# Optimization experiments

Measured on AMD Instinct MI355X. Metric: run time of the kernel, lower is better.

## Reference

```python
import jax, jax.numpy as jnp
import numpy as np

EPS_DEN = 1e-7
EPS_SQRT = 1e-12  # clamp before sqrt (torch.cdist matmul-mode also clamps at 0)


def setup_inputs() -> dict:
    key = jax.random.key(0)
    k1, k2 = jax.random.split(key)
    L, N, Q, C = 6, 256, 64, 256
    hs_pair = jax.random.normal(k1, (L, N, Q, C), dtype=jnp.float32)
    centers = jax.random.normal(k2, (L, N, 2, C), dtype=jnp.float32)
    return {"hs_pair": hs_pair, "centers": centers}


def reference(hs_pair, centers):
    # hs_pair: [L, N, Q, C], centers: [L, N, 2, C]
    L, N, Q, C = hs_pair.shape
    x2 = jnp.sum(hs_pair * hs_pair, axis=-1)  # [L, N, Q], constant over iters

    def body(carry, _):
        cen, _prev_a = carry
        c2 = jnp.sum(cen * cen, axis=-1)                     # [L, N, 2]
        xc = jnp.einsum('lnqc,lnkc->lnqk', hs_pair, cen)     # [L, N, Q, 2]
        d2 = x2[..., None] + c2[:, :, None, :] - 2.0 * xc
        dist = jnp.sqrt(jnp.maximum(d2, EPS_SQRT))           # euclidean cdist
        a = jax.nn.softmax(-dist, axis=-1)                   # [L, N, Q, 2]
        num = jnp.einsum('lnqk,lnqc->lnkc', a, hs_pair)      # [L, N, 2, C]
        den = jnp.sum(a, axis=2)                             # [L, N, 2]
        new_cen = num / (den[..., None] + EPS_DEN)
        return (new_cen, a), None

    init_a = jnp.zeros((L, N, Q, 2), dtype=hs_pair.dtype)
    # Q sequential EM iterations; final assignment is the one computed from
    # the centers *before* the last update (matches the torch loop order).
    (centers_out, assignment), _ = jax.lax.scan(body, (centers, init_a), None, length=Q)
    return centers_out, assignment
```

## Files before the change

kernel.cpp:

```cpp
#include <hip/hip_runtime.h>

namespace {
constexpr int PB = 6 * 256;
constexpr int Q = 64;
constexpr int C = 256;
constexpr float EPS_DEN = 1e-7f;
constexpr float EPS_SQRT = 1e-12f;
constexpr int GT_FLOATS = Q * Q;
constexpr int AUX_FLOATS = 256;

typedef __attribute__((ext_vector_type(8))) short bf16x8;
typedef __attribute__((ext_vector_type(4))) float f32x4;

template <int CTRL>
__device__ __forceinline__ float ror_add(float v) {
  int r = __builtin_amdgcn_mov_dpp(__float_as_int(v), CTRL, 0xF, 0xF, true);
  return v + __int_as_float(r);
}

__device__ __forceinline__ float wave_total(float v) {
  v = ror_add<0x121>(v);
  v = ror_add<0x122>(v);
  v = ror_add<0x124>(v);
  v = ror_add<0x128>(v);
  {
    int t = __builtin_amdgcn_update_dpp(0, __float_as_int(v), 0x142, 0xA, 0xF,
                                        true);
    v = v + __int_as_float(t);
  }
  {
    int t = __builtin_amdgcn_update_dpp(0, __float_as_int(v), 0x143, 0xC, 0xF,
                                        true);
    v = v + __int_as_float(t);
  }
  return __int_as_float(__builtin_amdgcn_readlane(__float_as_int(v), 63));
}

__device__ __forceinline__ ushort bf16_rne(float x) {
  uint u = __float_as_uint(x);
  return (ushort)((u + 0x7FFFu + ((u >> 16) & 1u)) >> 16);
}
__device__ __forceinline__ float bf16_up(ushort h) {
  return __uint_as_float((uint)h << 16);
}

__device__ __forceinline__ void wave_fence() { asm volatile("" ::: "memory"); }
}

__global__ __launch_bounds__(256, 2) void k1_gram(
    const float* __restrict__ hs, const float* __restrict__ cen,
    float* __restrict__ ws) {
  const int prob = blockIdx.x;
  const int tid = threadIdx.x;
  const int lane = tid & 63, w = tid >> 6;
  const int li = lane & 15, lk = lane >> 4;

  __shared__ __align__(16) ushort Hh[64 * 128];
  __shared__ __align__(16) ushort Hl[64 * 128];
  __shared__ __align__(16) ushort Ch[2 * 256];
  __shared__ __align__(16) ushort Cl[2 * 256];

  const float4* hsg4 = (const float4*)(hs + (size_t)prob * Q * C);
  float* gtp = ws + (size_t)prob * GT_FLOATS;
  float* aux = ws + (size_t)PB * GT_FLOATS + (size_t)prob * AUX_FLOATS;

  f32x4 acc[4] = {{0.f, 0.f, 0.f, 0.f},
                  {0.f, 0.f, 0.f, 0.f},
                  {0.f, 0.f, 0.f, 0.f},
                  {0.f, 0.f, 0.f, 0.f}};
  f32x4 accX = {0.f, 0.f, 0.f, 0.f};
  const int rA = 16 * w + li;
  const int swz = (li & 7) << 4;

#pragma unroll 1
  for (int half = 0; half < 2; ++half) {
#pragma unroll
    for (int i = 0; i < 8; ++i) {
      const int c = i * 256 + tid;
      const int r = c >> 5, col4 = c & 31;
      float4 v = hsg4[r * 64 + half * 32 + col4];
      ushort h0 = bf16_rne(v.x), h1 = bf16_rne(v.y), h2 = bf16_rne(v.z),
             h3 = bf16_rne(v.w);
      ushort l0 = bf16_rne(v.x - bf16_up(h0));
      ushort l1 = bf16_rne(v.y - bf16_up(h1));
      ushort l2 = bf16_rne(v.z - bf16_up(h2));
      ushort l3 = bf16_rne(v.w - bf16_up(h3));
      const int boff = (col4 * 8) ^ ((r & 7) << 4);
      const int idx = r * 128 + (boff >> 1);
      *(ushort4*)&Hh[idx] = make_ushort4(h0, h1, h2, h3);
      *(ushort4*)&Hl[idx] = make_ushort4(l0, l1, l2, l3);
    }
    if (half == 0) {
      if (tid < 128) {
        const float4* cg4 = (const float4*)(cen + (size_t)prob * 2 * C);
        float4 v = cg4[tid];
        ushort h0 = bf16_rne(v.x), h1 = bf16_rne(v.y), h2 = bf16_rne(v.z),
               h3 = bf16_rne(v.w);
        ushort l0 = bf16_rne(v.x - bf16_up(h0));
        ushort l1 = bf16_rne(v.y - bf16_up(h1));
        ushort l2 = bf16_rne(v.z - bf16_up(h2));
        ushort l3 = bf16_rne(v.w - bf16_up(h3));
        const int idx = (tid >> 6) * 256 + (tid & 63) * 4;
        *(ushort4*)&Ch[idx] = make_ushort4(h0, h1, h2, h3);
        *(ushort4*)&Cl[idx] = make_ushort4(l0, l1, l2, l3);
      }
      float c0v = cen[(size_t)prob * 2 * C + tid];
      float c1v = cen[(size_t)prob * 2 * C + C + tid];
      float p0 = wave_total(c0v * c0v);
      float p1 = wave_total(c1v * c1v);
      if (lane == 0) {
        aux[192 + w] = p0;
        aux[196 + w] = p1;
      }
    }
    __syncthreads();

#pragma unroll
    for (int kk2 = 0; kk2 < 4; ++kk2) {
      const int kk = half * 4 + kk2;
      const int byteA = (kk2 * 64 + lk * 16) ^ swz;
      const int offA = byteA >> 1;
      bf16x8 ah = *(const bf16x8*)&Hh[rA * 128 + offA];
      bf16x8 al = *(const bf16x8*)&Hl[rA * 128 + offA];
      bf16x8 cbh = {0, 0, 0, 0, 0, 0, 0, 0};
      bf16x8 cbl = {0, 0, 0, 0, 0, 0, 0, 0};
      if (li < 2) {
        const int cidx = li * 256 + kk * 32 + lk * 8;
        cbh = *(const bf16x8*)&Ch[cidx];
        cbl = *(const bf16x8*)&Cl[cidx];
      }
      accX = __builtin_amdgcn_mfma_f32_16x16x32_bf16(ah, cbh, accX, 0, 0, 0);
      accX = __builtin_amdgcn_mfma_f32_16x16x32_bf16(ah, cbl, accX, 0, 0, 0);
      accX = __builtin_amdgcn_mfma_f32_16x16x32_bf16(al, cbh, accX, 0, 0, 0);
#pragma unroll
      for (int tj = 0; tj < 4; ++tj) {
        if (tj < w) continue;
        const int rB = 16 * tj + li;
        bf16x8 bh = *(const bf16x8*)&Hh[rB * 128 + offA];
        bf16x8 bl = *(const bf16x8*)&Hl[rB * 128 + offA];
        acc[tj] =
            __builtin_amdgcn_mfma_f32_16x16x32_bf16(ah, bh, acc[tj], 0, 0, 0);
        acc[tj] =
            __builtin_amdgcn_mfma_f32_16x16x32_bf16(ah, bl, acc[tj], 0, 0, 0);
        acc[tj] =
            __builtin_amdgcn_mfma_f32_16x16x32_bf16(al, bh, acc[tj], 0, 0, 0);
      }
    }
    __syncthreads();
  }

#pragma unroll
  for (int tj = 0; tj < 4; ++tj) {
    if (tj < w) continue;
#pragma unroll
    for (int r = 0; r < 4; ++r) {
      const float v = acc[tj][r];
      const int row = 16 * w + lk * 4 + r;
      const int col = 16 * tj + li;
      gtp[(col >> 2) * 256 + row * 4 + (col & 3)] = v;
      if (tj > w) gtp[(row >> 2) * 256 + col * 4 + (row & 3)] = v;
      if (row == col) aux[128 + row] = v;
    }
  }
  if (li < 2) {
#pragma unroll
    for (int r = 0; r < 4; ++r) {
      const int q = 16 * w + lk * 4 + r;
      aux[q * 2 + li] = accX[r];
    }
  }
}

__global__ __launch_bounds__(64, 2) void k2_iter(const float* __restrict__ hs,
                                                 const float* __restrict__ ws,
                                                 float* __restrict__ out) {
  const int prob = blockIdx.x;
  const int lane = threadIdx.x;
  const int li = lane & 15, lk = lane >> 4;

  __shared__ __align__(16) ushort Ah[2][64];
  __shared__ __align__(16) float m_s[2][64];
  __shared__ __align__(16) float a_s[2 * Q];

  const float4* gt4 = (const float4*)(ws + (size_t)prob * GT_FLOATS);
  const float* aux = ws + (size_t)PB * GT_FLOATS + (size_t)prob * AUX_FLOATS;

  bf16x8 Gh[4][2], Gl[4][2];
#pragma unroll
  for (int t = 0; t < 4; ++t) {
#pragma unroll
    for (int kk = 0; kk < 2; ++kk) {
      const int cj = 8 * kk + 2 * lk;
      float4 ga = gt4[cj * 64 + 16 * t + li];
      float4 gb = gt4[(cj + 1) * 64 + 16 * t + li];
      float g[8] = {ga.x, ga.y, ga.z, ga.w, gb.x, gb.y, gb.z, gb.w};
      bf16x8 hh, ll;
#pragma unroll
      for (int j = 0; j < 8; ++j) {
        ushort h = bf16_rne(g[j]);
        hh[j] = (short)h;
        ll[j] = (short)bf16_rne(g[j] - bf16_up(h));
      }
      Gh[t][kk] = hh;
      Gl[t][kk] = ll;
    }
  }

  const float x2 = aux[128 + lane];
  float xc0 = aux[lane * 2 + 0];
  float xc1 = aux[lane * 2 + 1];
  float c20 = aux[192] + aux[193] + aux[194] + aux[195];
  float c21 = aux[196] + aux[197] + aux[198] + aux[199];

  float a0 = 0.f, a1 = 0.f;
  const int cl = li & 1;

#pragma unroll 1
  for (int t = 0; t < Q; ++t) {
    float d0 = fmaxf(x2 + c20 - 2.f * xc0, EPS_SQRT);
    float d1 = fmaxf(x2 + c21 - 2.f * xc1, EPS_SQRT);
    float t0 = __builtin_amdgcn_sqrtf(d0), t1 = __builtin_amdgcn_sqrtf(d1);
    float e0 = __expf(-t0), e1 = __expf(-t1);
    float inv = __builtin_amdgcn_rcpf(e0 + e1);
    a0 = e0 * inv;
    a1 = e1 * inv;
    if (t == Q - 1) break;

    Ah[0][lane] = bf16_rne(a0);
    Ah[1][lane] = bf16_rne(a1);
    float den0 = wave_total(a0);
    float den1 = wave_total(a1);
    wave_fence();

    bf16x8 bh[2];
#pragma unroll
    for (int kk = 0; kk < 2; ++kk)
      bh[kk] = *(const bf16x8*)&Ah[cl][kk * 32 + lk * 8];

    f32x4 acc[4] = {{0.f, 0.f, 0.f, 0.f},
                    {0.f, 0.f, 0.f, 0.f},
                    {0.f, 0.f, 0.f, 0.f},
                    {0.f, 0.f, 0.f, 0.f}};
#pragma unroll
    for (int tt = 0; tt < 4; ++tt) {
#pragma unroll
      for (int kk = 0; kk < 2; ++kk) {
        acc[tt] = __builtin_amdgcn_mfma_f32_16x16x32_bf16(Gh[tt][kk], bh[kk],
                                                          acc[tt], 0, 0, 0);
        acc[tt] = __builtin_amdgcn_mfma_f32_16x16x32_bf16(Gl[tt][kk], bh[kk],
                                                          acc[tt], 0, 0, 0);
      }
    }
    if (li < 2) {
#pragma unroll
      for (int tt = 0; tt < 4; ++tt)
        *(float4*)&m_s[li][16 * tt + lk * 4] =
            make_float4(acc[tt][0], acc[tt][1], acc[tt][2], acc[tt][3]);
    }
    wave_fence();

    float m0 = m_s[0][lane];
    float m1 = m_s[1][lane];
    float s0 = wave_total(a0 * m0);
    float s1 = wave_total(a1 * m1);

    float i0 = __builtin_amdgcn_rcpf(den0 + EPS_DEN);
    float i1 = __builtin_amdgcn_rcpf(den1 + EPS_DEN);
    xc0 = m0 * i0;
    xc1 = m1 * i1;
    c20 = s0 * i0 * i0;
    c21 = s1 * i1 * i1;
  }

  *(float2*)&a_s[lane * 2] = make_float2(a0, a1);
  float den0 = wave_total(a0);
  float den1 = wave_total(a1);
  wave_fence();
  float i0 = __builtin_amdgcn_rcpf(den0 + EPS_DEN);
  float i1 = __builtin_amdgcn_rcpf(den1 + EPS_DEN);

  const float4* hb4 = (const float4*)(hs + (size_t)prob * Q * C);
  const float2* a2 = (const float2*)a_s;
  float4 n0 = make_float4(0.f, 0.f, 0.f, 0.f);
  float4 n1 = make_float4(0.f, 0.f, 0.f, 0.f);
#pragma unroll 8
  for (int q2 = 0; q2 < Q; ++q2) {
    float4 h = hb4[q2 * 64 + lane];
    float2 aq = a2[q2];
    n0.x = fmaf(aq.x, h.x, n0.x);
    n0.y = fmaf(aq.x, h.y, n0.y);
    n0.z = fmaf(aq.x, h.z, n0.z);
    n0.w = fmaf(aq.x, h.w, n0.w);
    n1.x = fmaf(aq.y, h.x, n1.x);
    n1.y = fmaf(aq.y, h.y, n1.y);
    n1.z = fmaf(aq.y, h.z, n1.z);
    n1.w = fmaf(aq.y, h.w, n1.w);
  }
  float4* outc4 = (float4*)(out + (size_t)prob * 2 * C);
  outc4[lane] = make_float4(n0.x * i0, n0.y * i0, n0.z * i0, n0.w * i0);
  outc4[64 + lane] = make_float4(n1.x * i1, n1.y * i1, n1.z * i1, n1.w * i1);

  float* outa = out + (size_t)PB * 2 * C + (size_t)prob * Q * 2;
  *(float2*)&outa[lane * 2] = make_float2(a0, a1);
}

extern "C" void kernel_launch(void* const* d_in, const int* in_sizes, int n_in,
                              void* d_out, int out_size, void* d_ws,
                              size_t ws_size, hipStream_t stream) {
  const float* hs = (const float*)d_in[0];
  const float* cen = (const float*)d_in[1];
  float* out = (float*)d_out;
  float* ws = (float*)d_ws;
  hipLaunchKernelGGL(k1_gram, dim3(PB), dim3(256), 0, stream, hs, cen, ws);
  hipLaunchKernelGGL(k2_iter, dim3(PB), dim3(64), 0, stream, hs, ws, out);
}
```

Before: 81.14 us.

## Load Gram-kernel MFMA operands directly from global memory, dropping LDS staging

```diff
diff --git a/kernel.cpp b/kernel.cpp
--- a/kernel.cpp
+++ b/kernel.cpp
@@ -44,6 +44,17 @@
   return __uint_as_float((uint)h << 16);
 }
 
+__device__ __forceinline__ void cvt8(float4 x, float4 y, bf16x8& hh,
+                                     bf16x8& ll) {
+  float v[8] = {x.x, x.y, x.z, x.w, y.x, y.y, y.z, y.w};
+#pragma unroll
+  for (int j = 0; j < 8; ++j) {
+    ushort h = bf16_rne(v[j]);
+    hh[j] = (short)h;
+    ll[j] = (short)bf16_rne(v[j] - bf16_up(h));
+  }
+}
+
 __device__ __forceinline__ void wave_fence() { asm volatile("" ::: "memory"); }
 }
 
@@ -55,14 +66,21 @@
   const int lane = tid & 63, w = tid >> 6;
   const int li = lane & 15, lk = lane >> 4;
 
-  __shared__ __align__(16) ushort Hh[64 * 128];
-  __shared__ __align__(16) ushort Hl[64 * 128];
-  __shared__ __align__(16) ushort Ch[2 * 256];
-  __shared__ __align__(16) ushort Cl[2 * 256];
-
-  const float4* hsg4 = (const float4*)(hs + (size_t)prob * Q * C);
+  const float* __restrict__ hsb = hs + (size_t)prob * Q * C;
+  const float* __restrict__ cenb = cen + (size_t)prob * 2 * C;
   float* gtp = ws + (size_t)prob * GT_FLOATS;
   float* aux = ws + (size_t)PB * GT_FLOATS + (size_t)prob * AUX_FLOATS;
+
+  {
+    float c0v = cenb[tid];
+    float c1v = cenb[C + tid];
+    float p0 = wave_total(c0v * c0v);
+    float p1 = wave_total(c1v * c1v);
+    if (lane == 0) {
+      aux[192 + w] = p0;
+      aux[196 + w] = p1;
+    }
+  }
 
   f32x4 acc[4] = {{0.f, 0.f, 0.f, 0.f},
                   {0.f, 0.f, 0.f, 0.f},
@@ -70,83 +88,42 @@
                   {0.f, 0.f, 0.f, 0.f}};
   f32x4 accX = {0.f, 0.f, 0.f, 0.f};
   const int rA = 16 * w + li;
-  const int swz = (li & 7) << 4;
-
-#pragma unroll 1
-  for (int half = 0; half < 2; ++half) {
-#pragma unroll
-    for (int i = 0; i < 8; ++i) {
-      const int c = i * 256 + tid;
-      const int r = c >> 5, col4 = c & 31;
-      float4 v = hsg4[r * 64 + half * 32 + col4];
-      ushort h0 = bf16_rne(v.x), h1 = bf16_rne(v.y), h2 = bf16_rne(v.z),
-             h3 = bf16_rne(v.w);
-      ushort l0 = bf16_rne(v.x - bf16_up(h0));
-      ushort l1 = bf16_rne(v.y - bf16_up(h1));
-      ushort l2 = bf16_rne(v.z - bf16_up(h2));
-      ushort l3 = bf16_rne(v.w - bf16_up(h3));
-      const int boff = (col4 * 8) ^ ((r & 7) << 4);
-      const int idx = r * 128 + (boff >> 1);
-      *(ushort4*)&Hh[idx] = make_ushort4(h0, h1, h2, h3);
-      *(ushort4*)&Hl[idx] = make_ushort4(l0, l1, l2, l3);
-    }
-    if (half == 0) {
-      if (tid < 128) {
-        const float4* cg4 = (const float4*)(cen + (size_t)prob * 2 * C);
-        float4 v = cg4[tid];
-        ushort h0 = bf16_rne(v.x), h1 = bf16_rne(v.y), h2 = bf16_rne(v.z),
-               h3 = bf16_rne(v.w);
-        ushort l0 = bf16_rne(v.x - bf16_up(h0));
-        ushort l1 = bf16_rne(v.y - bf16_up(h1));
-        ushort l2 = bf16_rne(v.z - bf16_up(h2));
-        ushort l3 = bf16_rne(v.w - bf16_up(h3));
-        const int idx = (tid >> 6) * 256 + (tid & 63) * 4;
-        *(ushort4*)&Ch[idx] = make_ushort4(h0, h1, h2, h3);
-        *(ushort4*)&Cl[idx] = make_ushort4(l0, l1, l2, l3);
-      }
-      float c0v = cen[(size_t)prob * 2 * C + tid];
-      float c1v = cen[(size_t)prob * 2 * C + C + tid];
-      float p0 = wave_total(c0v * c0v);
-      float p1 = wave_total(c1v * c1v);
-      if (lane == 0) {
-        aux[192 + w] = p0;
-        aux[196 + w] = p1;
-      }
-    }
-    __syncthreads();
-
-#pragma unroll
-    for (int kk2 = 0; kk2 < 4; ++kk2) {
-      const int kk = half * 4 + kk2;
-      const int byteA = (kk2 * 64 + lk * 16) ^ swz;
-      const int offA = byteA >> 1;
-      bf16x8 ah = *(const bf16x8*)&Hh[rA * 128 + offA];
-      bf16x8 al = *(const bf16x8*)&Hl[rA * 128 + offA];
-      bf16x8 cbh = {0, 0, 0, 0, 0, 0, 0, 0};
-      bf16x8 cbl = {0, 0, 0, 0, 0, 0, 0, 0};
-      if (li < 2) {
-        const int cidx = li * 256 + kk * 32 + lk * 8;
-        cbh = *(const bf16x8*)&Ch[cidx];
-        cbl = *(const bf16x8*)&Cl[cidx];
-      }
-      accX = __builtin_amdgcn_mfma_f32_16x16x32_bf16(ah, cbh, accX, 0, 0, 0);
-      accX = __builtin_amdgcn_mfma_f32_16x16x32_bf16(ah, cbl, accX, 0, 0, 0);
-      accX = __builtin_amdgcn_mfma_f32_16x16x32_bf16(al, cbh, accX, 0, 0, 0);
-#pragma unroll
-      for (int tj = 0; tj < 4; ++tj) {
-        if (tj < w) continue;
-        const int rB = 16 * tj + li;
-        bf16x8 bh = *(const bf16x8*)&Hh[rB * 128 + offA];
-        bf16x8 bl = *(const bf16x8*)&Hl[rB * 128 + offA];
-        acc[tj] =
-            __builtin_amdgcn_mfma_f32_16x16x32_bf16(ah, bh, acc[tj], 0, 0, 0);
-        acc[tj] =
-            __builtin_amdgcn_mfma_f32_16x16x32_bf16(ah, bl, acc[tj], 0, 0, 0);
-        acc[tj] =
-            __builtin_amdgcn_mfma_f32_16x16x32_bf16(al, bh, acc[tj], 0, 0, 0);
-      }
-    }
-    __syncthreads();
+  const int kbase = lk * 8;
+
+#pragma unroll
+  for (int kk = 0; kk < 8; ++kk) {
+    const int kcol = kk * 32 + kbase;
+    const float* pa = hsb + rA * C + kcol;
+    bf16x8 ah, al;
+    cvt8(*(const float4*)pa, *(const float4*)(pa + 4), ah, al);
+
+    bf16x8 cbh = {0, 0, 0, 0, 0, 0, 0, 0};
+    bf16x8 cbl = {0, 0, 0, 0, 0, 0, 0, 0};
+    if (li < 2) {
+      const float* pc = cenb + li * C + kcol;
+      cvt8(*(const float4*)pc, *(const float4*)(pc + 4), cbh, cbl);
+    }
+    accX = __builtin_amdgcn_mfma_f32_16x16x32_bf16(ah, cbh, accX, 0, 0, 0);
+    accX = __builtin_amdgcn_mfma_f32_16x16x32_bf16(ah, cbl, accX, 0, 0, 0);
+    accX = __builtin_amdgcn_mfma_f32_16x16x32_bf16(al, cbh, accX, 0, 0, 0);
+
+    acc[w] = __builtin_amdgcn_mfma_f32_16x16x32_bf16(ah, ah, acc[w], 0, 0, 0);
+    acc[w] = __builtin_amdgcn_mfma_f32_16x16x32_bf16(ah, al, acc[w], 0, 0, 0);
+    acc[w] = __builtin_amdgcn_mfma_f32_16x16x32_bf16(al, ah, acc[w], 0, 0, 0);
+
+#pragma unroll
+    for (int tj = 0; tj < 4; ++tj) {
+      if (tj <= w) continue;
+      const float* pb = hsb + (16 * tj + li) * C + kcol;
+      bf16x8 bh, bl;
+      cvt8(*(const float4*)pb, *(const float4*)(pb + 4), bh, bl);
+      acc[tj] =
+          __builtin_amdgcn_mfma_f32_16x16x32_bf16(ah, bh, acc[tj], 0, 0, 0);
+      acc[tj] =
+          __builtin_amdgcn_mfma_f32_16x16x32_bf16(ah, bl, acc[tj], 0, 0, 0);
+      acc[tj] =
+          __builtin_amdgcn_mfma_f32_16x16x32_bf16(al, bh, acc[tj], 0, 0, 0);
+    }
   }
 
 #pragma unroll
```

After: 106.2 us. 1.31x slower.
